# Performance work log

Measured on AMD Instinct MI355X. Metric: run time of the kernel, lower is better.

Reference implementation:

```python
import jax, jax.numpy as jnp
import numpy as np
import math

B, S, DM, H, DH = 2, 2048, 1024, 16, 64  # batch, seq, d_model, heads, head_dim


def setup_inputs() -> dict:
    key = jax.random.key(0)
    ks = jax.random.split(key, 4)
    scale = 0.02
    return {
        "hidden_states": jax.random.normal(ks[0], (B, S, DM), jnp.float32),
        "Wq": jax.random.normal(ks[1], (DM, DM), jnp.float32) * scale,
        "bq": jnp.zeros((DM,), jnp.float32),
        "Wk": jax.random.normal(ks[2], (DM, DM), jnp.float32) * scale,
        "bk": jnp.zeros((DM,), jnp.float32),
        "Wv": jax.random.normal(ks[3], (DM, DM), jnp.float32) * scale,
        "bv": jnp.zeros((DM,), jnp.float32),
    }


def reference(hidden_states, Wq, bq, Wk, bk, Wv, bv):
    b, s, _ = hidden_states.shape

    def proj(W, bias):
        # torch Linear: x @ W.T + b, then transpose_for_scores -> [B,H,S,Dh]
        x = hidden_states @ W.T + bias
        return x.reshape(b, s, H, DH).transpose(0, 2, 1, 3)

    query = proj(Wq, bq)
    key = proj(Wk, bk)
    value = proj(Wv, bv)

    # qk_matmul input calibration stats (abs-max over whole tensor)
    q_max = jax.lax.stop_gradient(jnp.max(jnp.abs(query)))
    kT_max = jax.lax.stop_gradient(jnp.max(jnp.abs(key)))  # transpose doesn't change abs-max

    attn_weights = jnp.einsum('bhqd,bhkd->bhqk', query, key)  # [B,H,S,S]
    qk_out_max = jax.lax.stop_gradient(jnp.max(jnp.abs(attn_weights)))

    attn_weights = attn_weights / math.sqrt(DH)
    attn_weights = jax.nn.softmax(attn_weights.astype(jnp.float32), axis=-1).astype(query.dtype)
    # eval mode: dropout p=0.0; head_mask is None

    # v_matmul input stats; note source also records attn_weights abs-max as 'v_matmul_out' (faithful)
    aw_max = jax.lax.stop_gradient(jnp.max(jnp.abs(attn_weights)))
    v_max = jax.lax.stop_gradient(jnp.max(jnp.abs(value)))
    v_out_max = aw_max  # source bug: re-reads attn_weights for v_matmul_out

    attn_output = jnp.einsum('bhqk,bhkd->bhqd', attn_weights, value)
    attn_output = attn_output.transpose(0, 2, 1, 3).reshape(b, s, H * DH)
    return attn_output, q_max, kT_max, qk_out_max, aw_max, v_max, v_out_max
```

## Files before the change

kernel.cpp:

```cpp
#include <hip/hip_runtime.h>
#include <hip/hip_bf16.h>
#include <stdint.h>

typedef __attribute__((ext_vector_type(8))) short short8;
typedef __attribute__((ext_vector_type(4))) short short4v;
typedef __attribute__((ext_vector_type(4))) float f32x4;

#define MFMA(a, b, c) __builtin_amdgcn_mfma_f32_16x16x32_bf16((a), (b), (c), 0, 0, 0)

#define C1 0.18033688011112042f
#define INV_C1 5.545177444479562f

static __device__ __forceinline__ unsigned int f2bf2(float x, float y) {
  union { __hip_bfloat162 h; unsigned int u; } c;
  c.h = __float22bfloat162_rn(make_float2(x, y));
  return c.u;
}

static __device__ __forceinline__ float exp2_fast(float x) {
  float r;
  asm("v_exp_f32 %0, %1" : "=v"(r) : "v"(x));
  return r;
}
static __device__ __forceinline__ unsigned int cvtpk(float lo, float hi) {
  unsigned int r;
  asm("v_cvt_pk_bf16_f32 %0, %1, %2" : "=v"(r) : "v"(lo), "v"(hi));
  return r;
}

static __device__ __forceinline__ void atomic_max_f32(float* addr, float v) {
  atomicMax((int*)addr, __float_as_int(v));
}

static __device__ __forceinline__ void gl_lds16(const void* g, void* l) {
  __builtin_amdgcn_global_load_lds(
      (const __attribute__((address_space(1))) void*)g,
      (__attribute__((address_space(3))) void*)l, 16, 0, 0);
}

__global__ __launch_bounds__(256) void k_cvt(
    const float* __restrict__ X, const float* __restrict__ Wq,
    const float* __restrict__ Wk, const float* __restrict__ Wv,
    short* __restrict__ Xb, short* __restrict__ Wb) {
  const int y = blockIdx.y;
  const int i = (blockIdx.x * 256 + threadIdx.x) * 8;
  const float* src;
  short* dstbase;
  if (y == 0) {
    if (i >= 4096 * 1024) return;
    src = X;
    dstbase = Xb;
  } else {
    if (i >= 1048576) return;
    src = (y == 1) ? Wq : (y == 2) ? Wk : Wv;
    dstbase = Wb + (y - 1) * 1048576;
  }
  const float4 a = *(const float4*)(src + i);
  const float4 b = *(const float4*)(src + i + 4);
  union { unsigned int u[4]; short8 s; } P;
  P.u[0] = f2bf2(a.x, a.y);
  P.u[1] = f2bf2(a.z, a.w);
  P.u[2] = f2bf2(b.x, b.y);
  P.u[3] = f2bf2(b.z, b.w);
  const int s = i >> 10, c0 = i & 1023;
  const int off = (((s >> 7) * 32 + (c0 >> 5)) * 4 + ((c0 >> 3) & 3)) * 1024 +
                  (s & 127) * 8;
  *(short8*)(dstbase + off) = P.s;
}

__global__ __launch_bounds__(256) void k_qkv(
    const short* __restrict__ Xb, const short* __restrict__ Wball,
    const float* __restrict__ bq, const float* __restrict__ bk,
    const float* __restrict__ bv,
    short* __restrict__ Qo, short* __restrict__ Ko, short* __restrict__ Vo,
    float* __restrict__ stats) {
  const int fid = (blockIdx.z * 32 + blockIdx.y) * 8 + blockIdx.x;
  const int sid = (fid & 7) * 96 + (fid >> 3);
  const int colb = sid & 7;
  const int zy = sid >> 3;
  const int z = zy >> 5;
  const int yb = zy & 31;

  const float* bias = (z == 0) ? bq : (z == 1) ? bk : bv;
  short* out = (z == 0) ? Qo : (z == 1) ? Ko : Vo;
  const bool qk = (z < 2);

  __shared__ __align__(16) short B0s[8192];
  __shared__ __align__(16) short B1s[8192];
  __shared__ __align__(16) short B2s[8192];
  __shared__ float red[4];

  const int t = threadIdx.x;
  const int lane = t & 63;
  const int w = t >> 6;
  const int l16 = lane & 15, quad = lane >> 4;
  const int wr = (w >> 1) * 64, wc = (w & 1) * 64;
  const int row0 = yb * 128;
  const int col0 = colb * 128;

  const short* ag = Xb + yb * 131072 + w * 512 + lane * 8;
  const short* bg = Wball + z * 1048576 + colb * 131072 + w * 512 + lane * 8;

  const int f0b = qk ? 4096 : 0, f0r = qk ? wc : wr;
  const int f1b = qk ? 0 : 4096, f1r = qk ? wr : wc;
  const int cq = quad * 1024;

  f32x4 acc[4][4];
#pragma unroll
  for (int i = 0; i < 4; ++i)
#pragma unroll
    for (int j = 0; j < 4; ++j) acc[i][j] = {0.f, 0.f, 0.f, 0.f};

#define STAGE(buf, ko_)                                  \
  do {                                                   \
    gl_lds16(ag + (ko_), (buf) + w * 512);               \
    gl_lds16(ag + (ko_) + 2048, (buf) + 2048 + w * 512); \
    gl_lds16(bg + (ko_), (buf) + 4096 + w * 512);        \
    gl_lds16(bg + (ko_) + 2048, (buf) + 6144 + w * 512); \
  } while (0)

#define COMPUTE(buf)                                                   \
  do {                                                                 \
    short8 fr0[4], fr1[4];                                             \
    _Pragma("unroll") for (int a = 0; a < 4; ++a)                      \
        fr0[a] = *(const short8*)&(buf)[f0b + cq + (f0r + a * 16 + l16) * 8]; \
    _Pragma("unroll") for (int b = 0; b < 4; ++b)                      \
        fr1[b] = *(const short8*)&(buf)[f1b + cq + (f1r + b * 16 + l16) * 8]; \
    _Pragma("unroll") for (int a = 0; a < 4; ++a)                      \
        _Pragma("unroll") for (int b = 0; b < 4; ++b)                  \
            acc[a][b] = MFMA(fr0[a], fr1[b], acc[a][b]);               \
  } while (0)

#define WAITBAR(n)                                                          \
  do {                                                                      \
    asm volatile("s_waitcnt lgkmcnt(0) vmcnt(" #n ")\n\ts_barrier" ::: "memory"); \
    __builtin_amdgcn_sched_barrier(0);                                      \
  } while (0)

  STAGE(B0s, 0);
  STAGE(B1s, 4096);
  WAITBAR(4);
  int ks = 8192;
#pragma unroll
  for (int i = 0; i < 10; ++i) {
    STAGE(B2s, ks); ks += 4096; COMPUTE(B0s); WAITBAR(4);
    STAGE(B0s, ks); ks += 4096; COMPUTE(B1s); WAITBAR(4);
    STAGE(B1s, ks); ks += 4096; COMPUTE(B2s); WAITBAR(4);
  }
  COMPUTE(B0s);
  WAITBAR(0);
  COMPUTE(B1s);
#undef STAGE
#undef COMPUTE
#undef WAITBAR

  float amax = 0.f;
  if (z == 0) {
#pragma unroll
    for (int a = 0; a < 4; ++a) {
      const int dg = col0 + wc + a * 16 + quad * 4;
      const float4 b4 = *(const float4*)&bias[dg];
      const int h = dg >> 6, dl = dg & 63;
#pragma unroll
      for (int b = 0; b < 4; ++b) {
        const int sg = row0 + wr + b * 16 + l16;
        const float y0 = acc[a][b][0] + b4.x;
        const float y1 = acc[a][b][1] + b4.y;
        const float y2 = acc[a][b][2] + b4.z;
        const float y3 = acc[a][b][3] + b4.w;
        amax = fmaxf(amax, fmaxf(fmaxf(fabsf(y0), fabsf(y1)), fmaxf(fabsf(y2), fabsf(y3))));
        union { unsigned int u[2]; short4v s; } pk;
        pk.u[0] = cvtpk(y0 * C1, y1 * C1);
        pk.u[1] = cvtpk(y2 * C1, y3 * C1);
        const int bidx = sg >> 11, sl = sg & 2047;
        *(short4v*)&out[(size_t)((((bidx << 4) | h) * 2048 + sl)) * 64 + dl] = pk.s;
      }
    }
  } else if (z == 1) {
#pragma unroll
    for (int a = 0; a < 4; ++a) {
      const int dg = col0 + wc + a * 16 + quad * 4;
      const float4 b4 = *(const float4*)&bias[dg];
      const int h = dg >> 6, dl = dg & 63;
#pragma unroll
      for (int b = 0; b < 4; ++b) {
        const int sg = row0 + wr + b * 16 + l16;
        const float y0 = acc[a][b][0] + b4.x;
        const float y1 = acc[a][b][1] + b4.y;
        const float y2 = acc[a][b][2] + b4.z;
        const float y3 = acc[a][b][3] + b4.w;
        amax = fmaxf(amax, fmaxf(fmaxf(fabsf(y0), fabsf(y1)), fmaxf(fabsf(y2), fabsf(y3))));
        union { unsigned int u[2]; short4v s; } pk;
        pk.u[0] = cvtpk(y0, y1);
        pk.u[1] = cvtpk(y2, y3);
        const int bidx = sg >> 11, sl = sg & 2047;
        const int ktt = sl >> 6, row = sl & 63;
        const size_t tb = ((size_t)(((bidx << 4) | h) * 32 + ktt) * 64 + row) * 64;
        *(short4v*)&out[tb + (((dl >> 3) ^ (row & 7)) * 8) + (dl & 7)] = pk.s;
      }
    }
  } else {
#pragma unroll
    for (int a = 0; a < 4; ++a) {
      const int sg = row0 + wr + a * 16 + quad * 4;
      const int bidx = sg >> 11, sl = sg & 2047;
      const int ktt = sl >> 6, key = sl & 63;
#pragma unroll
      for (int b = 0; b < 4; ++b) {
        const int dg = col0 + wc + b * 16 + l16;
        const float bvf = bias[dg];
        const int h = dg >> 6, dl = dg & 63;
        const float y0 = acc[a][b][0] + bvf;
        const float y1 = acc[a][b][1] + bvf;
        const float y2 = acc[a][b][2] + bvf;
        const float y3 = acc[a][b][3] + bvf;
        amax = fmaxf(amax, fmaxf(fmaxf(fabsf(y0), fabsf(y1)), fmaxf(fabsf(y2), fabsf(y3))));
        union { unsigned int u[2]; short4v s; } pk;
        pk.u[0] = cvtpk(y0, y1);
        pk.u[1] = cvtpk(y2, y3);
        const size_t tb = ((size_t)(((bidx << 4) | h) * 32 + ktt) * 64 + dl) * 64;
        *(short4v*)&out[tb + (((key >> 3) ^ (dl & 7)) * 8) + (key & 7)] = pk.s;
      }
    }
  }
#pragma unroll
  for (int off = 32; off > 0; off >>= 1)
    amax = fmaxf(amax, __shfl_xor(amax, off, 64));
  if (lane == 0) red[w] = amax;
  __syncthreads();
  if (t == 0) {
    float m = fmaxf(fmaxf(red[0], red[1]), fmaxf(red[2], red[3]));
    atomic_max_f32(&stats[z], m);
  }
}

__global__ __launch_bounds__(512) void k_attn(
    const short* __restrict__ Q, const short* __restrict__ K,
    const short* __restrict__ V, float* __restrict__ O,
    float* __restrict__ stats) {
  const int fid = blockIdx.y * 16 + blockIdx.x;
  const int sid = ((fid & 7) << 6) + (fid >> 3);
  const int bh = sid >> 4;
  const int q0 = (sid & 15) << 7;
  const short* Qh = Q + (size_t)bh * 2048 * 64;

  __shared__ __align__(16) short Ks[3 * 4096];
  __shared__ __align__(16) short Vts[3 * 4096];
  __shared__ __align__(16) short Ps[8][16 * 64];
  __shared__ float redA[8], redB[8];

  const int t = threadIdx.x, lane = t & 63, w = t >> 6;
  const int l16 = lane & 15, quad = lane >> 4;
  const int rsw = (l16 & 7);
  short* myPs = &Ps[w][0];

  const short* kg = K + (size_t)bh * 131072 + w * 512 + lane * 8;
  const short* vg = V + (size_t)bh * 131072 + w * 512 + lane * 8;

  short8 bq0, bq1;
  {
    const short* qsrc = Qh + (q0 + w * 16 + l16) * 64 + quad * 8;
    bq0 = *(const short8*)qsrc;
    bq1 = *(const short8*)(qsrc + 32);
  }

  float m_lane = -1e30f, l_lane = 0.f, xmin_lane = 1e30f;
  f32x4 o_acc[4];
#pragma unroll
  for (int jn = 0; jn < 4; ++jn) o_acc[jn] = {0.f, 0.f, 0.f, 0.f};
  const f32x4 zero = {0.f, 0.f, 0.f, 0.f};

  const int ksl0 = (quad ^ rsw) * 8;
  const int ksl1 = ((quad ^ rsw) ^ 4) * 8;

#define ASTAGE(cb, ko_)                            \
  do {                                             \
    gl_lds16(kg + (ko_), Ks + (cb) * 4096 + w * 512);  \
    gl_lds16(vg + (ko_), Vts + (cb) * 4096 + w * 512); \
  } while (0)

#define AWAITBAR(n)                                                         \
  do {                                                                      \
    asm volatile("s_waitcnt lgkmcnt(0) vmcnt(" #n ")\n\ts_barrier" ::: "memory"); \
    __builtin_amdgcn_sched_barrier(0);                                      \
  } while (0)

#define ACOMPUTE(cb)                                                        \
  do {                                                                      \
    const int kbase = (cb) * 4096;                                          \
    f32x4 sacc[4];                                                          \
    __builtin_amdgcn_s_setprio(1);                                          \
    _Pragma("unroll") for (int j = 0; j < 4; ++j) {                         \
      const int kb = kbase + (j * 16 + l16) * 64;                           \
      short8 kf0 = *(const short8*)&Ks[kb + ksl0];                          \
      short8 kf1 = *(const short8*)&Ks[kb + ksl1];                          \
      sacc[j] = MFMA(kf1, bq1, MFMA(kf0, bq0, zero));                       \
    }                                                                       \
    __builtin_amdgcn_s_setprio(0);                                          \
    {                                                                       \
      float pmax = m_lane, psum = l_lane, xmn = xmin_lane;                  \
      _Pragma("unroll") for (int j = 0; j < 4; ++j) {                       \
        const float x0 = sacc[j][0], x1 = sacc[j][1];                       \
        const float x2 = sacc[j][2], x3 = sacc[j][3];                       \
        pmax = fmaxf(fmaxf(x0, fmaxf(x1, x2)), fmaxf(x3, pmax));            \
        xmn = fminf(fminf(x0, fminf(x1, x2)), fminf(x3, xmn));              \
        const float e0 = exp2_fast(x0), e1 = exp2_fast(x1);                 \
        const float e2 = exp2_fast(x2), e3 = exp2_fast(x3);                 \
        psum += (e0 + e1) + (e2 + e3);                                      \
        union { unsigned int u[2]; short4v s; } pk;                         \
        pk.u[0] = cvtpk(e0, e1);                                            \
        pk.u[1] = cvtpk(e2, e3);                                            \
        *(short4v*)&myPs[l16 * 64 + ((j * 16 + quad * 4) ^ (rsw << 3))] = pk.s; \
      }                                                                     \
      m_lane = pmax; l_lane = psum; xmin_lane = xmn;                        \
    }                                                                       \
    asm volatile("" ::: "memory");                                          \
    __builtin_amdgcn_s_setprio(1);                                          \
    _Pragma("unroll") for (int tstep = 0; tstep < 2; ++tstep) {             \
      const int psl = (tstep * 32 + quad * 8) ^ (rsw << 3);                 \
      short8 ap = *(const short8*)&myPs[l16 * 64 + psl];                    \
      _Pragma("unroll") for (int jn = 0; jn < 4; ++jn) {                    \
        short8 vf = *(const short8*)&Vts[kbase + (jn * 16 + l16) * 64 + psl]; \
        o_acc[jn] = MFMA(ap, vf, o_acc[jn]);                                \
      }                                                                     \
    }                                                                       \
    __builtin_amdgcn_s_setprio(0);                                          \
    asm volatile("" ::: "memory");                                          \
  } while (0)

  ASTAGE(0, 0);
  ASTAGE(1, 4096);
  AWAITBAR(2);
  int ko = 8192;
#pragma unroll
  for (int i = 0; i < 10; ++i) {
    ASTAGE(2, ko); ko += 4096; ACOMPUTE(0); AWAITBAR(2);
    ASTAGE(0, ko); ko += 4096; ACOMPUTE(1); AWAITBAR(2);
    ASTAGE(1, ko); ko += 4096; ACOMPUTE(2); AWAITBAR(2);
  }
  ACOMPUTE(0);
  AWAITBAR(0);
  ACOMPUTE(1);
#undef ASTAGE
#undef AWAITBAR
#undef ACOMPUTE

  float l = l_lane;
  l += __shfl_xor(l, 16, 64);
  l += __shfl_xor(l, 32, 64);
  float m = m_lane;
  m = fmaxf(m, __shfl_xor(m, 16, 64));
  m = fmaxf(m, __shfl_xor(m, 32, 64));
  float xm = xmin_lane;
  xm = fminf(xm, __shfl_xor(xm, 16, 64));
  xm = fminf(xm, __shfl_xor(xm, 32, 64));
  float aw = exp2_fast(m) / l;
  float qkx = fmaxf(m, -xm);

  const int bidx = bh >> 4, h = bh & 15;
  float linv[4];
#pragma unroll
  for (int r = 0; r < 4; ++r)
    linv[r] = 1.0f / __shfl(l, quad * 4 + r, 16);
#pragma unroll
  for (int jn = 0; jn < 4; ++jn) {
    const int d = jn * 16 + l16;
#pragma unroll
    for (int r = 0; r < 4; ++r) {
      const int s_row = q0 + w * 16 + quad * 4 + r;
      O[((size_t)(bidx * 2048 + s_row) * 1024) + h * 64 + d] =
          o_acc[jn][r] * linv[r];
    }
  }

#pragma unroll
  for (int off = 32; off > 0; off >>= 1) {
    qkx = fmaxf(qkx, __shfl_xor(qkx, off, 64));
    aw = fmaxf(aw, __shfl_xor(aw, off, 64));
  }
  if (lane == 0) {
    redA[w] = qkx;
    redB[w] = aw;
  }
  __syncthreads();
  if (t == 0) {
    float a = redA[0], b = redB[0];
#pragma unroll
    for (int i = 1; i < 8; ++i) {
      a = fmaxf(a, redA[i]);
      b = fmaxf(b, redB[i]);
    }
    atomic_max_f32(&stats[3], a * INV_C1);
    atomic_max_f32(&stats[4], b);
  }
}

__global__ void k_fin(const float* __restrict__ stats, float* __restrict__ out) {
  const int i = threadIdx.x;
  if (i == 0) out[0] = stats[0];
  if (i == 1) out[1] = stats[1];
  if (i == 2) out[2] = stats[3];
  if (i == 3) out[3] = stats[4];
  if (i == 4) out[4] = stats[2];
  if (i == 5) out[5] = stats[4];
}

extern "C" void kernel_launch(void* const* d_in, const int* in_sizes, int n_in,
                              void* d_out, int out_size, void* d_ws, size_t ws_size,
                              hipStream_t stream) {
  const float* X = (const float*)d_in[0];
  const float* Wq = (const float*)d_in[1];
  const float* bq = (const float*)d_in[2];
  const float* Wk = (const float*)d_in[3];
  const float* bk = (const float*)d_in[4];
  const float* Wv = (const float*)d_in[5];
  const float* bv = (const float*)d_in[6];
  float* out = (float*)d_out;

  float* stats = (float*)d_ws;
  short* base = (short*)((char*)d_ws + 4096);
  short* Qb = base;
  short* Kb = base + 4194304;
  short* Vb = base + 8388608;
  short* Xb = base + 12582912;
  short* Wb = base + 16777216;

  k_cvt<<<dim3(2048, 4), 256, 0, stream>>>(X, Wq, Wk, Wv, Xb, Wb);
  k_qkv<<<dim3(8, 32, 3), 256, 0, stream>>>(Xb, Wb, bq, bk, bv, Qb, Kb, Vb, stats);
  k_attn<<<dim3(16, 32), 512, 0, stream>>>(Qb, Kb, Vb, out, stats);
  k_fin<<<1, 64, 0, stream>>>(stats, out + 4194304);
}
```

Measured before the change: 177.4 us.

## Process two 16-row query groups per wave to reuse K/V tiles

Measured after the change: 180.4 us. About the same (+1.7%).

```diff
diff --git a/kernel.cpp b/kernel.cpp
--- a/kernel.cpp
+++ b/kernel.cpp
@@ -238,15 +238,15 @@
     const short* __restrict__ Q, const short* __restrict__ K,
     const short* __restrict__ V, float* __restrict__ O,
     float* __restrict__ stats) {
-  const int fid = blockIdx.y * 16 + blockIdx.x;
-  const int sid = ((fid & 7) << 6) + (fid >> 3);
-  const int bh = sid >> 4;
-  const int q0 = (sid & 15) << 7;
+  const int fid = blockIdx.y * 8 + blockIdx.x;
+  const int sid = ((fid & 7) << 5) + (fid >> 3);
+  const int bh = sid >> 3;
+  const int q0 = (sid & 7) << 8;
   const short* Qh = Q + (size_t)bh * 2048 * 64;
 
   __shared__ __align__(16) short Ks[3 * 4096];
   __shared__ __align__(16) short Vts[3 * 4096];
-  __shared__ __align__(16) short Ps[8][16 * 64];
+  __shared__ __align__(16) short Ps[8][32 * 64];
   __shared__ float redA[8], redB[8];
 
   const int t = threadIdx.x, lane = t & 63, w = t >> 6;
@@ -257,17 +257,21 @@
   const short* kg = K + (size_t)bh * 131072 + w * 512 + lane * 8;
   const short* vg = V + (size_t)bh * 131072 + w * 512 + lane * 8;
 
-  short8 bq0, bq1;
-  {
-    const short* qsrc = Qh + (q0 + w * 16 + l16) * 64 + quad * 8;
-    bq0 = *(const short8*)qsrc;
-    bq1 = *(const short8*)(qsrc + 32);
-  }
-
-  float m_lane = -1e30f, l_lane = 0.f, xmin_lane = 1e30f;
-  f32x4 o_acc[4];
-#pragma unroll
-  for (int jn = 0; jn < 4; ++jn) o_acc[jn] = {0.f, 0.f, 0.f, 0.f};
+  short8 bq8[2][2];
+#pragma unroll
+  for (int g = 0; g < 2; ++g) {
+    const short* qsrc = Qh + (q0 + w * 32 + g * 16 + l16) * 64 + quad * 8;
+    bq8[g][0] = *(const short8*)qsrc;
+    bq8[g][1] = *(const short8*)(qsrc + 32);
+  }
+
+  float m_lane[2] = {-1e30f, -1e30f}, l_lane[2] = {0.f, 0.f};
+  float xmin_lane[2] = {1e30f, 1e30f};
+  f32x4 o_acc[2][4];
+#pragma unroll
+  for (int g = 0; g < 2; ++g)
+#pragma unroll
+    for (int jn = 0; jn < 4; ++jn) o_acc[g][jn] = {0.f, 0.f, 0.f, 0.f};
   const f32x4 zero = {0.f, 0.f, 0.f, 0.f};
 
   const int ksl0 = (quad ^ rsw) * 8;
@@ -288,20 +292,21 @@
 #define ACOMPUTE(cb)                                                        \
   do {                                                                      \
     const int kbase = (cb) * 4096;                                          \
-    f32x4 sacc[4];                                                          \
+    f32x4 sacc[2][4];                                                       \
     __builtin_amdgcn_s_setprio(1);                                          \
     _Pragma("unroll") for (int j = 0; j < 4; ++j) {                         \
       const int kb = kbase + (j * 16 + l16) * 64;                           \
       short8 kf0 = *(const short8*)&Ks[kb + ksl0];                          \
       short8 kf1 = *(const short8*)&Ks[kb + ksl1];                          \
-      sacc[j] = MFMA(kf1, bq1, MFMA(kf0, bq0, zero));                       \
+      sacc[0][j] = MFMA(kf1, bq8[0][1], MFMA(kf0, bq8[0][0], zero));        \
+      sacc[1][j] = MFMA(kf1, bq8[1][1], MFMA(kf0, bq8[1][0], zero));        \
     }                                                                       \
     __builtin_amdgcn_s_setprio(0);                                          \
-    {                                                                       \
-      float pmax = m_lane, psum = l_lane, xmn = xmin_lane;                  \
+    _Pragma("unroll") for (int g = 0; g < 2; ++g) {                         \
+      float pmax = m_lane[g], psum = l_lane[g], xmn = xmin_lane[g];         \
       _Pragma("unroll") for (int j = 0; j < 4; ++j) {                       \
-        const float x0 = sacc[j][0], x1 = sacc[j][1];                       \
-        const float x2 = sacc[j][2], x3 = sacc[j][3];                       \
+        const float x0 = sacc[g][j][0], x1 = sacc[g][j][1];                 \
+        const float x2 = sacc[g][j][2], x3 = sacc[g][j][3];                 \
         pmax = fmaxf(fmaxf(x0, fmaxf(x1, x2)), fmaxf(x3, pmax));            \
         xmn = fminf(fminf(x0, fminf(x1, x2)), fminf(x3, xmn));              \
         const float e0 = exp2_fast(x0), e1 = exp2_fast(x1);                 \
@@ -310,18 +315,21 @@
         union { unsigned int u[2]; short4v s; } pk;                         \
         pk.u[0] = cvtpk(e0, e1);                                            \
         pk.u[1] = cvtpk(e2, e3);                                            \
-        *(short4v*)&myPs[l16 * 64 + ((j * 16 + quad * 4) ^ (rsw << 3))] = pk.s; \
+        *(short4v*)&myPs[(g * 16 + l16) * 64 +                              \
+                         ((j * 16 + quad * 4) ^ (rsw << 3))] = pk.s;        \
       }                                                                     \
-      m_lane = pmax; l_lane = psum; xmin_lane = xmn;                        \
+      m_lane[g] = pmax; l_lane[g] = psum; xmin_lane[g] = xmn;               \
     }                                                                       \
     asm volatile("" ::: "memory");                                          \
     __builtin_amdgcn_s_setprio(1);                                          \
     _Pragma("unroll") for (int tstep = 0; tstep < 2; ++tstep) {             \
       const int psl = (tstep * 32 + quad * 8) ^ (rsw << 3);                 \
-      short8 ap = *(const short8*)&myPs[l16 * 64 + psl];                    \
+      short8 ap0 = *(const short8*)&myPs[l16 * 64 + psl];                   \
+      short8 ap1 = *(const short8*)&myPs[(16 + l16) * 64 + psl];            \
       _Pragma("unroll") for (int jn = 0; jn < 4; ++jn) {                    \
         short8 vf = *(const short8*)&Vts[kbase + (jn * 16 + l16) * 64 + psl]; \
-        o_acc[jn] = MFMA(ap, vf, o_acc[jn]);                                \
+        o_acc[0][jn] = MFMA(ap0, vf, o_acc[0][jn]);                         \
+        o_acc[1][jn] = MFMA(ap1, vf, o_acc[1][jn]);                         \
       }                                                                     \
     }                                                                       \
     __builtin_amdgcn_s_setprio(0);                                          \
@@ -345,31 +353,43 @@
 #undef AWAITBAR
 #undef ACOMPUTE
 
-  float l = l_lane;
-  l += __shfl_xor(l, 16, 64);
-  l += __shfl_xor(l, 32, 64);
-  float m = m_lane;
-  m = fmaxf(m, __shfl_xor(m, 16, 64));
-  m = fmaxf(m, __shfl_xor(m, 32, 64));
-  float xm = xmin_lane;
-  xm = fminf(xm, __shfl_xor(xm, 16, 64));
-  xm = fminf(xm, __shfl_xor(xm, 32, 64));
-  float aw = exp2_fast(m) / l;
-  float qkx = fmaxf(m, -xm);
+  float l_full[2], m_full[2], xm_full[2];
+#pragma unroll
+  for (int g = 0; g < 2; ++g) {
+    float l = l_lane[g];
+    l += __shfl_xor(l, 16, 64);
+    l += __shfl_xor(l, 32, 64);
+    l_full[g] = l;
+    float m = m_lane[g];
+    m = fmaxf(m, __shfl_xor(m, 16, 64));
+    m = fmaxf(m, __shfl_xor(m, 32, 64));
+    m_full[g] = m;
+    float xm = xmin_lane[g];
+    xm = fminf(xm, __shfl_xor(xm, 16, 64));
+    xm = fminf(xm, __shfl_xor(xm, 32, 64));
+    xm_full[g] = xm;
+  }
+  float aw = fmaxf(exp2_fast(m_full[0]) / l_full[0],
+                   exp2_fast(m_full[1]) / l_full[1]);
+  float qkx = fmaxf(fmaxf(m_full[0], -xm_full[0]),
+                    fmaxf(m_full[1], -xm_full[1]));
 
   const int bidx = bh >> 4, h = bh & 15;
-  float linv[4];
-#pragma unroll
-  for (int r = 0; r < 4; ++r)
-    linv[r] = 1.0f / __shfl(l, quad * 4 + r, 16);
-#pragma unroll
-  for (int jn = 0; jn < 4; ++jn) {
-    const int d = jn * 16 + l16;
-#pragma unroll
-    for (int r = 0; r < 4; ++r) {
-      const int s_row = q0 + w * 16 + quad * 4 + r;
-      O[((size_t)(bidx * 2048 + s_row) * 1024) + h * 64 + d] =
-          o_acc[jn][r] * linv[r];
+#pragma unroll
+  for (int g = 0; g < 2; ++g) {
+    float linv[4];
+#pragma unroll
+    for (int r = 0; r < 4; ++r)
+      linv[r] = 1.0f / __shfl(l_full[g], quad * 4 + r, 16);
+#pragma unroll
+    for (int jn = 0; jn < 4; ++jn) {
+      const int d = jn * 16 + l16;
+#pragma unroll
+      for (int r = 0; r < 4; ++r) {
+        const int s_row = q0 + w * 32 + g * 16 + quad * 4 + r;
+        O[((size_t)(bidx * 2048 + s_row) * 1024) + h * 64 + d] =
+            o_acc[g][jn][r] * linv[r];
+      }
     }
   }
 
@@ -427,6 +447,6 @@
 
   k_cvt<<<dim3(2048, 4), 256, 0, stream>>>(X, Wq, Wk, Wv, Xb, Wb);
   k_qkv<<<dim3(8, 32, 3), 256, 0, stream>>>(Xb, Wb, bq, bk, bv, Qb, Kb, Vb, stats);
-  k_attn<<<dim3(16, 32), 512, 0, stream>>>(Qb, Kb, Vb, out, stats);
+  k_attn<<<dim3(8, 32), 512, 0, stream>>>(Qb, Kb, Vb, out, stats);
   k_fin<<<1, 64, 0, stream>>>(stats, out + 4194304);
 }
```
